# Kernel optimization log

Measured on AMD Instinct MI355X. Metric: run time of the kernel, lower is better.

The kernel has to match this reference:

```python
import jax, jax.numpy as jnp
import numpy as np

SIGMA = 1.0
DELTA = 1.0
TOPK = 10
TOPK_HALF = 5  # int(np.around(TOPK / 2))


def l2norm(x):
    # F.normalize: x / max(||x||, 1e-12)
    n = jnp.linalg.norm(x, axis=-1, keepdims=True)
    return x / jnp.maximum(n, 1e-12)


def cdist(a, b):
    # pairwise euclidean distance with grad-safe sqrt (0 on exact-zero dists)
    d2 = (jnp.sum(a * a, axis=1)[:, None] + jnp.sum(b * b, axis=1)[None, :]
          - 2.0 * a @ b.T)
    d2 = jnp.maximum(d2, 0.0)
    return jnp.where(d2 > 0.0, jnp.sqrt(jnp.where(d2 > 0.0, d2, 1.0)), 0.0)


def rc_weights(t_emb, idx):
    # all of this is under torch.no_grad() in the original
    N = t_emb.shape[0]
    T_dist = cdist(t_emb, t_emb)
    W_P = jnp.exp(-(T_dist ** 2) / SIGMA)
    same_id = idx[:, None] == idx[None, :]
    W_P_copy = jnp.where(same_id, 1.0, W_P)
    _, topk_index = jax.lax.top_k(W_P_copy, TOPK)            # [N, k]
    topk_half_index = topk_index[:, :TOPK_HALF]               # [N, k/2]
    rows = jnp.arange(N)[:, None]
    W_NN = jnp.zeros((N, N), W_P.dtype).at[rows, topk_index].set(1.0)
    V = (((W_NN + W_NN.T) / 2.0) == 1.0).astype(W_P.dtype)    # mutual-NN graph
    # vectorized form of the per-row loop:
    # W_C_tilda[i, j] = V[i, j] * |N(i) \cap N(j)| / |N(i)|
    deg = V.sum(axis=1)                                       # |N(i)| per row
    VV = V @ V                                                # V symmetric -> (V@V)[i,j] = |N(i) cap N(j)|
    W_C_tilda = jnp.where(V > 0.0, VV / jnp.maximum(deg, 1.0)[:, None], 0.0)
    W_C_hat = W_C_tilda[topk_half_index].mean(axis=1)         # [N, N]
    W_C = (W_C_hat + W_C_hat.T) / 2.0
    W = (W_P + W_C) / 2.0
    off_diag = 1.0 - jnp.eye(N, dtype=W.dtype)
    pos_weight = W * off_diag
    neg_weight = (1.0 - W) * off_diag
    return pos_weight, neg_weight


def rc_loss(s_emb, t_emb, idx):
    s_emb = l2norm(s_emb)        # disable_mu=True
    t_emb = l2norm(t_emb)
    N = s_emb.shape[0]
    S_dist = cdist(s_emb, s_emb)
    S_dist = S_dist / S_dist.mean(axis=1, keepdims=True)
    pos_w, neg_w = rc_weights(t_emb, idx)
    pos_w = jax.lax.stop_gradient(pos_w)
    neg_w = jax.lax.stop_gradient(neg_w)
    pull = jax.nn.relu(S_dist) ** 2 * pos_w
    push = jax.nn.relu(DELTA - S_dist) ** 2 * neg_w
    return (pull.sum() + push.sum()) / (N * (N - 1))


def kl_loss(s_f, s_g):
    # disable_mu=True -> normalize both
    s_f = l2norm(s_f)
    s_g = l2norm(s_g)
    N = s_f.shape[0]
    S_dist = cdist(s_f, s_f)
    S_dist = S_dist / S_dist.mean(axis=1, keepdims=True)
    S_bg = cdist(s_g, s_g)
    S_bg = S_bg / S_bg.mean(axis=1, keepdims=True)
    log_q = jax.nn.log_softmax(-S_dist, axis=-1)
    log_p = jax.nn.log_softmax(jax.lax.stop_gradient(-S_bg), axis=-1)
    p = jnp.exp(log_p)
    return jnp.sum(p * (log_p - log_q)) / N


def setup_inputs() -> dict:
    key = jax.random.key(0)
    k1, k2, k3, k4 = jax.random.split(key, 4)
    N = 4096
    s_f = jax.random.normal(k1, (N, 512), jnp.float32)
    s_g = jax.random.normal(k2, (N, 512), jnp.float32)
    t_g = jax.random.normal(k3, (N, 1024), jnp.float32)
    idx = jax.random.randint(k4, (N,), 0, 2048, jnp.int64 if jax.config.jax_enable_x64 else jnp.int32)
    return {"s_f": s_f, "s_g": s_g, "t_g": t_g, "idx": idx}


def reference(s_f, s_g, t_g, idx):
    loss_RC_f = rc_loss(s_f, t_g, idx)
    loss_RC_g = rc_loss(s_g, t_g, idx)
    loss_RC = (loss_RC_f + loss_RC_g) / 2.0
    loss_KL = kl_loss(s_f, s_g)
    return loss_RC, loss_KL, loss_RC + loss_KL
```

## Files before the change

### kernel.cpp

```cpp
#include <hip/hip_runtime.h>
#include <hip/hip_bf16.h>

#define NN 4096
typedef unsigned short u16;
typedef __bf16 bf16x8 __attribute__((ext_vector_type(8)));
typedef float f32x4 __attribute__((ext_vector_type(4)));
typedef u16 u16x8 __attribute__((ext_vector_type(8)));

typedef const __attribute__((address_space(1))) void* gptr_t;
typedef __attribute__((address_space(3))) void* lptr_t;

__device__ inline u16 bf16bits(float v) {
    __bf16 h = (__bf16)v;
    return __builtin_bit_cast(u16, h);
}
__device__ inline float bf16val(float v) {
    __bf16 h = (__bf16)v;
    return (float)h;
}
__device__ inline float b2f(u16 b) { return __uint_as_float(((unsigned)b) << 16); }

__device__ inline float block_sum(float v, volatile float* sbuf) {
    int lane = threadIdx.x & 63, wv = threadIdx.x >> 6;
#pragma unroll
    for (int o = 32; o > 0; o >>= 1) v += __shfl_xor(v, o, 64);
    if (lane == 0) sbuf[wv] = v;
    __syncthreads();
    float r = sbuf[0] + sbuf[1] + sbuf[2] + sbuf[3];
    __syncthreads();
    return r;
}

template <int D>
__global__ void normalize_kernel(const float* __restrict__ in, u16* __restrict__ outb,
                                 float* __restrict__ ssout) {
    __shared__ float sbuf[4];
    constexpr int NV = D / 4;
    int row = blockIdx.x, tid = threadIdx.x;
    const float4* x4 = (const float4*)(in + (size_t)row * D);
    float4 v = make_float4(0.f, 0.f, 0.f, 0.f);
    if (tid < NV) v = x4[tid];
    float s = v.x * v.x + v.y * v.y + v.z * v.z + v.w * v.w;
    float tot = block_sum(s, sbuf);
    float inv = 1.0f / fmaxf(sqrtf(tot), 1e-12f);
    float sb = 0.f;
    if (tid < NV) {
        float b0 = bf16val(v.x * inv), b1 = bf16val(v.y * inv);
        float b2 = bf16val(v.z * inv), b3 = bf16val(v.w * inv);
        ushort4 o;
        o.x = bf16bits(v.x * inv);
        o.y = bf16bits(v.y * inv);
        o.z = bf16bits(v.z * inv);
        o.w = bf16bits(v.w * inv);
        ((ushort4*)(outb + (size_t)row * D))[tid] = o;
        sb = b0 * b0 + b1 * b1 + b2 * b2 + b3 * b3;
    }
    float totb = block_sum(sb, sbuf);
    if (tid == 0) ssout[row] = totb;
}

#define TS 132
__launch_bounds__(256)
__global__ void gram_merged(const u16* __restrict__ tb, const u16* __restrict__ fb,
                            const u16* __restrict__ gb, const float* __restrict__ ss_t,
                            const float* __restrict__ ss_f, const float* __restrict__ ss_g,
                            u16* __restrict__ WP, u16* __restrict__ Sf, u16* __restrict__ Sg) {
    __shared__ __align__(16) u16 smem[16896];

    int bid = blockIdx.x;
    int seg = (bid < 528) ? 0 : (bid < 1056 ? 1 : 2);
    int p = bid - seg * 528;
    int l = (p & 7) * 66 + (p >> 3);
    int by = 0, rem = l;
    while (rem >= 32 - by) { rem -= 32 - by; ++by; }
    int bx = by + rem;

    const u16* X = (seg == 0) ? tb : (seg == 1 ? fb : gb);
    const float* ss = (seg == 0) ? ss_t : (seg == 1 ? ss_f : ss_g);
    u16* outp = (seg == 0) ? WP : (seg == 1 ? Sf : Sg);
    const int K = (seg == 0) ? 1024 : 512;
    const bool mode1 = (seg != 0);
    const bool offdiag = (bx != by);

    const int tid = threadIdx.x;
    const int wv = tid >> 6, lane = tid & 63;
    const int wr = wv >> 1, wc = wv & 1;
    const int brow = by * 128, bcol = bx * 128;
    const int r = lane & 15, kc = lane >> 4;
    const int crow = lane >> 2;
    const int koff = (lane & 3) * 8;

    f32x4 acc[4][4];
#pragma unroll
    for (int mi = 0; mi < 4; ++mi)
#pragma unroll
        for (int ni = 0; ni < 4; ++ni) acc[mi][ni] = (f32x4){0.f, 0.f, 0.f, 0.f};

    auto STAGE = [&](int buf, int k0) {
#pragma unroll
        for (int cc = 0; cc < 2; ++cc) {
            int c = wv * 2 + cc;
            const u16* ga = X + (size_t)(brow + c * 16 + crow) * K + k0 + koff;
            const u16* gbp = X + (size_t)(bcol + c * 16 + crow) * K + k0 + koff;
            __builtin_amdgcn_global_load_lds((gptr_t)ga, (lptr_t)&smem[buf * 4096 + c * 512], 16, 0, 0);
            __builtin_amdgcn_global_load_lds((gptr_t)gbp, (lptr_t)&smem[8192 + buf * 4096 + c * 512], 16, 0, 0);
        }
    };

    const int NT = K / 32;
    STAGE(0, 0);
    asm volatile("s_waitcnt vmcnt(0)" ::: "memory");
    __builtin_amdgcn_sched_barrier(0);
    __builtin_amdgcn_s_barrier();
    for (int t = 0; t < NT; ++t) {
        int cur = t & 1;
        if (t + 1 < NT) STAGE(cur ^ 1, (t + 1) * 32);

        bf16x8 af[4], bfr[4];
#pragma unroll
        for (int mi = 0; mi < 4; ++mi)
            af[mi] = *(const bf16x8*)&smem[cur * 4096 + (wr * 64 + mi * 16 + r) * 32 + kc * 8];
#pragma unroll
        for (int ni = 0; ni < 4; ++ni)
            bfr[ni] = *(const bf16x8*)&smem[8192 + cur * 4096 + (wc * 64 + ni * 16 + r) * 32 + kc * 8];

        asm volatile("s_waitcnt lgkmcnt(0)" ::: "memory");
        __builtin_amdgcn_sched_barrier(0);

#pragma unroll
        for (int mi = 0; mi < 4; ++mi)
#pragma unroll
            for (int ni = 0; ni < 4; ++ni)
                acc[mi][ni] = __builtin_amdgcn_mfma_f32_16x16x32_bf16(af[mi], bfr[ni], acc[mi][ni], 0, 0, 0);

        asm volatile("s_waitcnt vmcnt(0)" ::: "memory");
        __builtin_amdgcn_sched_barrier(0);
        __builtin_amdgcn_s_barrier();
    }
    __syncthreads();

    u16* tile = smem;
    const int q = lane >> 4;
#pragma unroll
    for (int mi = 0; mi < 4; ++mi) {
#pragma unroll
        for (int v = 0; v < 4; ++v) {
            int rl = wr * 64 + mi * 16 + q * 4 + v;
            float ssi = ss[brow + rl];
#pragma unroll
            for (int ni = 0; ni < 4; ++ni) {
                int cl = wc * 64 + ni * 16 + r;
                float d2 = fmaxf(ssi + ss[bcol + cl] - 2.0f * acc[mi][ni][v], 0.f);
                float o = mode1 ? sqrtf(d2) : __expf(-d2);
                tile[rl * TS + cl] = bf16bits(o);
            }
        }
    }
    __syncthreads();

    {
        int rl = tid >> 1, hf = tid & 1;
        const u16* srow = &tile[rl * TS + hf * 64];
        u16* drow = outp + (size_t)(brow + rl) * NN + bcol + hf * 64;
#pragma unroll
        for (int i = 0; i < 8; ++i) {
            ushort4 aa = *(const ushort4*)(srow + i * 8);
            ushort4 bb = *(const ushort4*)(srow + i * 8 + 4);
            u16x8 pk = {aa.x, aa.y, aa.z, aa.w, bb.x, bb.y, bb.z, bb.w};
            *(u16x8*)(drow + i * 8) = pk;
        }
    }

    if (offdiag) {
        int c = tid >> 1, hf = tid & 1;
        u16* drow = outp + (size_t)(bcol + c) * NN + brow + hf * 64;
#pragma unroll
        for (int s = 0; s < 8; ++s) {
            u16 g[8];
#pragma unroll
            for (int u = 0; u < 8; ++u) g[u] = tile[(hf * 64 + s * 8 + u) * TS + c];
            u16x8 pk = {g[0], g[1], g[2], g[3], g[4], g[5], g[6], g[7]};
            *(u16x8*)(drow + s * 8) = pk;
        }
    }
}

__global__ void topk_kernel(const u16* __restrict__ WP, const int* __restrict__ idx,
                            int* __restrict__ topk) {
    __shared__ unsigned long long sred[4];
    __shared__ unsigned long long sbest;
    int row = blockIdx.x, tid = threadIdx.x;
    int myid = idx[row];
    const u16x8* W8 = (const u16x8*)(WP + (size_t)row * NN);
    const int4* idx4 = (const int4*)idx;
    unsigned key[16];
#pragma unroll
    for (int a = 0; a < 2; ++a) {
        u16x8 w = W8[a * 256 + tid];
        int4 iA = idx4[a * 512 + tid * 2];
        int4 iB = idx4[a * 512 + tid * 2 + 1];
        int ids[8] = {iA.x, iA.y, iA.z, iA.w, iB.x, iB.y, iB.z, iB.w};
#pragma unroll
        for (int c = 0; c < 8; ++c)
            key[a * 8 + c] = (ids[c] == myid) ? 0x3F800000u : (((unsigned)w[c]) << 16);
    }
    int lane = tid & 63, wv = tid >> 6;
    for (int it = 0; it < 10; ++it) {
        unsigned long long best = 0;
#pragma unroll
        for (int a = 0; a < 2; ++a)
#pragma unroll
            for (int c = 0; c < 8; ++c) {
                unsigned j = (unsigned)(a * 2048 + tid * 8 + c);
                unsigned long long pk =
                    ((unsigned long long)key[a * 8 + c] << 32) | (0xFFFFFFFFu - j);
                if (pk > best) best = pk;
            }
#pragma unroll
        for (int o = 32; o > 0; o >>= 1) {
            unsigned long long t = __shfl_xor(best, o, 64);
            if (t > best) best = t;
        }
        if (lane == 0) sred[wv] = best;
        __syncthreads();
        if (tid == 0) {
            unsigned long long b = sred[0];
            for (int w2 = 1; w2 < 4; ++w2)
                if (sred[w2] > b) b = sred[w2];
            sbest = b;
        }
        __syncthreads();
        unsigned jstar = 0xFFFFFFFFu - (unsigned)(sbest & 0xFFFFFFFFu);
        if (tid == 0) topk[row * 10 + it] = (int)jstar;
        if (((jstar >> 3) & 255u) == (unsigned)tid) {
            unsigned slot = ((jstar >> 11) << 3) | (jstar & 7u);
#pragma unroll
            for (int a = 0; a < 16; ++a)
                if ((unsigned)a == slot) key[a] = 0u;
        }
        __syncthreads();
    }
}

__global__ void mutual_kernel(const int* __restrict__ topk, int* __restrict__ nbr,
                              int* __restrict__ deg) {
    int gid = blockIdx.x * 256 + threadIdx.x;
    if (gid >= NN * 10) return;
    int i = gid / 10, a = gid - i * 10;
    int j = topk[i * 10 + a];
    bool mut = false;
#pragma unroll
    for (int b = 0; b < 10; ++b) mut = mut || (topk[j * 10 + b] == i);
    nbr[gid] = mut ? j : -1;
    if (mut) atomicAdd(&deg[i], 1);
}

__global__ void tilda_kernel(const int* __restrict__ nbr, const int* __restrict__ deg,
                             float* __restrict__ tvals) {
    int gid = blockIdx.x * 256 + threadIdx.x;
    if (gid >= NN * 10) return;
    int m = gid / 10;
    int j = nbr[gid];
    if (j < 0) { tvals[gid] = 0.f; return; }
    int am[10], aj[10];
#pragma unroll
    for (int p = 0; p < 10; ++p) am[p] = nbr[m * 10 + p];
#pragma unroll
    for (int p = 0; p < 10; ++p) aj[p] = nbr[j * 10 + p];
    int cnt = 0;
#pragma unroll
    for (int p = 0; p < 10; ++p)
#pragma unroll
        for (int qq = 0; qq < 10; ++qq)
            cnt += (am[p] >= 0 && am[p] == aj[qq]) ? 1 : 0;
    int dm = deg[m];
    float dv = (float)(dm > 1 ? dm : 1);
    tvals[gid] = (float)cnt / dv;
}

__global__ void hat_kernel(const int* __restrict__ topk, const int* __restrict__ nbr,
                           const float* __restrict__ tvals, int* __restrict__ hcols,
                           float* __restrict__ hvals) {
    int gid = blockIdx.x * 256 + threadIdx.x;
    if (gid >= NN * 5) return;
    int i = gid / 5, h = gid - i * 5;
    int m = topk[i * 10 + h];
#pragma unroll
    for (int a = 0; a < 10; ++a) {
        int j = nbr[m * 10 + a];
        int slot = i * 50 + h * 10 + a;
        hcols[slot] = j;
        hvals[slot] = (j >= 0) ? tvals[m * 10 + a] * 0.2f : 0.f;
    }
}

__global__ void fused_dense_kernel(const u16* __restrict__ Sf, const u16* __restrict__ Sg,
                                   const u16* __restrict__ WP, float* __restrict__ rsf,
                                   float* __restrict__ rsg, double* __restrict__ acc) {
    __shared__ float sbuf[4];
    int row = blockIdx.x, tid = threadIdx.x;
    const u16x8* f8 = (const u16x8*)(Sf + (size_t)row * NN);
    const u16x8* g8 = (const u16x8*)(Sg + (size_t)row * NN);
    const u16x8* w8 = (const u16x8*)(WP + (size_t)row * NN);
    u16x8 fr[2], gr[2];
#pragma unroll
    for (int a = 0; a < 2; ++a) {
        fr[a] = f8[a * 256 + tid];
        gr[a] = g8[a * 256 + tid];
    }
    float sf_ = 0.f, sg_ = 0.f;
#pragma unroll
    for (int a = 0; a < 2; ++a)
#pragma unroll
        for (int c = 0; c < 8; ++c) {
            sf_ += b2f(fr[a][c]);
            sg_ += b2f(gr[a][c]);
        }
    float rsum_f = block_sum(sf_, sbuf);
    float rsum_g = block_sum(sg_, sbuf);
    if (tid == 0) {
        rsf[row] = rsum_f;
        rsg[row] = rsum_g;
    }
    float imf = (float)NN / rsum_f;
    float img = (float)NN / rsum_g;
    float vf[16], vg[16];
#pragma unroll
    for (int a = 0; a < 2; ++a)
#pragma unroll
        for (int c = 0; c < 8; ++c) {
            vf[a * 8 + c] = b2f(fr[a][c]) * imf;
            vg[a * 8 + c] = b2f(gr[a][c]) * img;
        }
    float ef = 0.f, eg = 0.f;
#pragma unroll
    for (int a = 0; a < 16; ++a) {
        ef += __expf(-vf[a]);
        eg += __expf(-vg[a]);
    }
    float lf = logf(block_sum(ef, sbuf));
    float lg = logf(block_sum(eg, sbuf));
    u16x8 wr2[2];
#pragma unroll
    for (int a = 0; a < 2; ++a) wr2[a] = w8[a * 256 + tid];
    float af = 0.f, ag = 0.f, akl = 0.f;
#pragma unroll
    for (int a = 0; a < 2; ++a) {
#pragma unroll
        for (int c = 0; c < 8; ++c) {
            int j = a * 2048 + tid * 8 + c;
            float wp = b2f(wr2[a][c]);
            float sf = vf[a * 8 + c], sg = vg[a * 8 + c];
            if (j != row) {
                float t = fmaxf(1.f - sf, 0.f);
                float pu = t * t;
                float gq = sf * sf - pu;
                af += pu + 0.5f * gq * wp;
                t = fmaxf(1.f - sg, 0.f);
                pu = t * t;
                gq = sg * sg - pu;
                ag += pu + 0.5f * gq * wp;
            }
            float lq = -sf - lf;
            float lp = -sg - lg;
            float pp = __expf(lp);
            akl += pp * (lp - lq);
        }
    }
    float tf = block_sum(af, sbuf);
    float tg2 = block_sum(ag, sbuf);
    float tk = block_sum(akl, sbuf);
    if (tid == 0) {
        int bank = (row & 63) * 8;
        atomicAdd(&acc[bank + 0], (double)tf);
        atomicAdd(&acc[bank + 1], (double)tg2);
        atomicAdd(&acc[bank + 2], (double)tk);
    }
}

__global__ void sparse_kernel(const u16* __restrict__ Sf, const u16* __restrict__ Sg,
                              const int* __restrict__ hcols, const float* __restrict__ hvals,
                              const float* __restrict__ rsf, const float* __restrict__ rsg,
                              double* __restrict__ acc) {
    __shared__ float sbuf[4];
    int lane = threadIdx.x & 63, wv = threadIdx.x >> 6;
    int i = blockIdx.x * 4 + wv;
    float cf = 0.f, cg = 0.f;
    if (lane < 50) {
        int j = hcols[i * 50 + lane];
        if (j >= 0 && j != i) {
            float v = hvals[i * 50 + lane];
            float imfi = (float)NN / rsf[i];
            float imgi = (float)NN / rsg[i];
            float s1 = b2f(Sf[(size_t)i * NN + j]) * imfi;
            float s2 = b2f(Sf[(size_t)j * NN + i]) * ((float)NN / rsf[j]);
            float t1 = fmaxf(1.f - s1, 0.f), t2 = fmaxf(1.f - s2, 0.f);
            cf = v * ((s1 * s1 - t1 * t1) + (s2 * s2 - t2 * t2));
            s1 = b2f(Sg[(size_t)i * NN + j]) * imgi;
            s2 = b2f(Sg[(size_t)j * NN + i]) * ((float)NN / rsg[j]);
            t1 = fmaxf(1.f - s1, 0.f);
            t2 = fmaxf(1.f - s2, 0.f);
            cg = v * ((s1 * s1 - t1 * t1) + (s2 * s2 - t2 * t2));
        }
    }
    float tf = block_sum(cf, sbuf);
    float tg = block_sum(cg, sbuf);
    if (threadIdx.x == 0) {
        int bank = (blockIdx.x & 63) * 8;
        atomicAdd(&acc[bank + 0], (double)(0.25f * tf));
        atomicAdd(&acc[bank + 1], (double)(0.25f * tg));
    }
}

__global__ void finalize_kernel(const double* __restrict__ acc, float* __restrict__ out) {
    if (threadIdx.x == 0) {
        double a0 = 0.0, a1 = 0.0, a2 = 0.0;
        for (int b = 0; b < 64; ++b) {
            a0 += acc[b * 8 + 0];
            a1 += acc[b * 8 + 1];
            a2 += acc[b * 8 + 2];
        }
        double denom = (double)NN * (double)(NN - 1);
        double rcf = a0 / denom, rcg = a1 / denom;
        double rc = 0.5 * (rcf + rcg);
        double kl = a2 / (double)NN;
        out[0] = (float)rc;
        out[1] = (float)kl;
        out[2] = (float)(rc + kl);
    }
}

extern "C" void kernel_launch(void* const* d_in, const int* in_sizes, int n_in, void* d_out,
                              int out_size, void* d_ws, size_t ws_size, hipStream_t stream) {
    const float* s_f = (const float*)d_in[0];
    const float* s_g = (const float*)d_in[1];
    const float* t_g = (const float*)d_in[2];
    const int* idx = (const int*)d_in[3];
    float* out = (float*)d_out;

    char* base = (char*)d_ws;
    size_t off = 0;
    auto alloc = [&](size_t b) {
        char* p = base + off;
        off = (off + b + 255) & ~(size_t)255;
        return p;
    };
    double* acc = (double*)alloc(64 * 8 * 8);
    int* deg = (int*)alloc(NN * 4);
    size_t zero_bytes = off;
    float* rowsum_f = (float*)alloc(NN * 4);
    float* rowsum_g = (float*)alloc(NN * 4);
    u16* tb = (u16*)alloc((size_t)NN * 1024 * 2);
    u16* fb = (u16*)alloc((size_t)NN * 512 * 2);
    u16* gb = (u16*)alloc((size_t)NN * 512 * 2);
    float* ss_t = (float*)alloc(NN * 4);
    float* ss_f = (float*)alloc(NN * 4);
    float* ss_g = (float*)alloc(NN * 4);
    u16* WP = (u16*)alloc((size_t)NN * NN * 2);
    u16* Sf = (u16*)alloc((size_t)NN * NN * 2);
    u16* Sg = (u16*)alloc((size_t)NN * NN * 2);
    int* topk = (int*)alloc(NN * 10 * 4);
    int* nbr = (int*)alloc(NN * 10 * 4);
    float* tvals = (float*)alloc(NN * 10 * 4);
    int* hcols = (int*)alloc(NN * 50 * 4);
    float* hvals = (float*)alloc(NN * 50 * 4);

    hipMemsetAsync(d_ws, 0, zero_bytes, stream);

    normalize_kernel<1024><<<NN, 256, 0, stream>>>(t_g, tb, ss_t);
    normalize_kernel<512><<<NN, 256, 0, stream>>>(s_f, fb, ss_f);
    normalize_kernel<512><<<NN, 256, 0, stream>>>(s_g, gb, ss_g);

    gram_merged<<<1584, 256, 0, stream>>>(tb, fb, gb, ss_t, ss_f, ss_g, WP, Sf, Sg);

    topk_kernel<<<NN, 256, 0, stream>>>(WP, idx, topk);
    mutual_kernel<<<(NN * 10 + 255) / 256, 256, 0, stream>>>(topk, nbr, deg);
    tilda_kernel<<<(NN * 10 + 255) / 256, 256, 0, stream>>>(nbr, deg, tvals);
    hat_kernel<<<(NN * 5 + 255) / 256, 256, 0, stream>>>(topk, nbr, tvals, hcols, hvals);

    fused_dense_kernel<<<NN, 256, 0, stream>>>(Sf, Sg, WP, rowsum_f, rowsum_g, acc);
    sparse_kernel<<<NN / 4, 256, 0, stream>>>(Sf, Sg, hcols, hvals, rowsum_f, rowsum_g, acc);
    finalize_kernel<<<1, 64, 0, stream>>>(acc, out);
}
```

Measured before the change: 206.3 us.

## Load Gram MFMA operands directly from global memory instead of LDS staging

Removes the double-buffered global_load_lds staging pipeline and barriers from the Gram kernel. Each lane now reads its bf16x8 MFMA fragments straight from global memory with an unrolled k-loop, and LDS is used only for the epilogue tile. This cuts LDS traffic and block-wide barriers, but drops cross-wave sharing of A/B tiles, so global/L2 traffic rises and load latency is no longer hidden by explicit prefetch.

```diff
diff --git a/kernel.cpp b/kernel.cpp
--- a/kernel.cpp
+++ b/kernel.cpp
@@ -6,9 +6,6 @@
 typedef __bf16 bf16x8 __attribute__((ext_vector_type(8)));
 typedef float f32x4 __attribute__((ext_vector_type(4)));
 typedef u16 u16x8 __attribute__((ext_vector_type(8)));
-
-typedef const __attribute__((address_space(1))) void* gptr_t;
-typedef __attribute__((address_space(3))) void* lptr_t;
 
 __device__ inline u16 bf16bits(float v) {
     __bf16 h = (__bf16)v;
@@ -65,7 +62,7 @@
                             const u16* __restrict__ gb, const float* __restrict__ ss_t,
                             const float* __restrict__ ss_f, const float* __restrict__ ss_g,
                             u16* __restrict__ WP, u16* __restrict__ Sf, u16* __restrict__ Sg) {
-    __shared__ __align__(16) u16 smem[16896];
+    __shared__ __align__(16) u16 tile[128 * TS];
 
     int bid = blockIdx.x;
     int seg = (bid < 528) ? 0 : (bid < 1056 ? 1 : 2);
@@ -87,8 +84,6 @@
     const int wr = wv >> 1, wc = wv & 1;
     const int brow = by * 128, bcol = bx * 128;
     const int r = lane & 15, kc = lane >> 4;
-    const int crow = lane >> 2;
-    const int koff = (lane & 3) * 8;
 
     f32x4 acc[4][4];
 #pragma unroll
@@ -96,50 +91,29 @@
 #pragma unroll
         for (int ni = 0; ni < 4; ++ni) acc[mi][ni] = (f32x4){0.f, 0.f, 0.f, 0.f};
 
-    auto STAGE = [&](int buf, int k0) {
-#pragma unroll
-        for (int cc = 0; cc < 2; ++cc) {
-            int c = wv * 2 + cc;
-            const u16* ga = X + (size_t)(brow + c * 16 + crow) * K + k0 + koff;
-            const u16* gbp = X + (size_t)(bcol + c * 16 + crow) * K + k0 + koff;
-            __builtin_amdgcn_global_load_lds((gptr_t)ga, (lptr_t)&smem[buf * 4096 + c * 512], 16, 0, 0);
-            __builtin_amdgcn_global_load_lds((gptr_t)gbp, (lptr_t)&smem[8192 + buf * 4096 + c * 512], 16, 0, 0);
-        }
-    };
-
-    const int NT = K / 32;
-    STAGE(0, 0);
-    asm volatile("s_waitcnt vmcnt(0)" ::: "memory");
-    __builtin_amdgcn_sched_barrier(0);
-    __builtin_amdgcn_s_barrier();
-    for (int t = 0; t < NT; ++t) {
-        int cur = t & 1;
-        if (t + 1 < NT) STAGE(cur ^ 1, (t + 1) * 32);
-
+    const u16* abase[4];
+    const u16* bbase[4];
+#pragma unroll
+    for (int mi = 0; mi < 4; ++mi)
+        abase[mi] = X + (size_t)(brow + wr * 64 + mi * 16 + r) * K + kc * 8;
+#pragma unroll
+    for (int ni = 0; ni < 4; ++ni)
+        bbase[ni] = X + (size_t)(bcol + wc * 64 + ni * 16 + r) * K + kc * 8;
+
+#pragma unroll 4
+    for (int k0 = 0; k0 < K; k0 += 32) {
         bf16x8 af[4], bfr[4];
 #pragma unroll
-        for (int mi = 0; mi < 4; ++mi)
-            af[mi] = *(const bf16x8*)&smem[cur * 4096 + (wr * 64 + mi * 16 + r) * 32 + kc * 8];
-#pragma unroll
-        for (int ni = 0; ni < 4; ++ni)
-            bfr[ni] = *(const bf16x8*)&smem[8192 + cur * 4096 + (wc * 64 + ni * 16 + r) * 32 + kc * 8];
-
-        asm volatile("s_waitcnt lgkmcnt(0)" ::: "memory");
-        __builtin_amdgcn_sched_barrier(0);
-
+        for (int mi = 0; mi < 4; ++mi) af[mi] = *(const bf16x8*)(abase[mi] + k0);
+#pragma unroll
+        for (int ni = 0; ni < 4; ++ni) bfr[ni] = *(const bf16x8*)(bbase[ni] + k0);
 #pragma unroll
         for (int mi = 0; mi < 4; ++mi)
 #pragma unroll
             for (int ni = 0; ni < 4; ++ni)
                 acc[mi][ni] = __builtin_amdgcn_mfma_f32_16x16x32_bf16(af[mi], bfr[ni], acc[mi][ni], 0, 0, 0);
-
-        asm volatile("s_waitcnt vmcnt(0)" ::: "memory");
-        __builtin_amdgcn_sched_barrier(0);
-        __builtin_amdgcn_s_barrier();
-    }
-    __syncthreads();
-
-    u16* tile = smem;
+    }
+
     const int q = lane >> 4;
 #pragma unroll
     for (int mi = 0; mi < 4; ++mi) {
```

Result: slower. 293.6 us (+42.3%).
